# Kernel optimization log

Hardware: AMD Instinct MI355X
Metric: run time of the kernel (lower is better)

Reference implementation:

```python
import jax, jax.numpy as jnp
import numpy as np

IN_SIZE, OUT_SIZE, EDGE_SIZE = 32, 32, 16
NET_LAYERS = [128, 128]          # cfg.net_layers (hidden sizes of the edge MLP)
B, N_NEIGH = 10000, 20           # nodes x neighbors
E = B * N_NEIGH                  # total edges


def setup_inputs() -> dict:
    key = jax.random.key(0)
    ks = jax.random.split(key, 16)
    h_v = jax.random.normal(ks[0], (B, N_NEIGH), jnp.float32)
    h_w = jax.random.normal(ks[1], (B, IN_SIZE), jnp.float32)
    e_vw = jax.random.normal(ks[2], (E, EDGE_SIZE), jnp.float32)
    dims = [EDGE_SIZE] + NET_LAYERS + [IN_SIZE * OUT_SIZE]
    params = {}
    for i, (din, dout) in enumerate(zip(dims[:-1], dims[1:])):
        bound = 1.0 / np.sqrt(din)  # torch nn.Linear default init
        params[f"W{i}"] = jax.random.uniform(ks[3 + 2 * i], (dout, din), jnp.float32, -bound, bound)
        params[f"b{i}"] = jax.random.uniform(ks[4 + 2 * i], (dout,), jnp.float32, -bound, bound)
    return {"h_v": h_v, "h_w": h_w, "e_vw": e_vw, **params}


def reference(h_v, h_w, e_vw, W0, b0, W1, b1, W2, b2):
    # Edge MLP: edge_size -> 128 -> 128 -> in*out (ReLU on hidden layers only)
    x = jax.nn.relu(e_vw @ W0.T + b0)
    x = jax.nn.relu(x @ W1.T + b1)
    m = (x @ W2.T + b2).reshape(-1, OUT_SIZE, IN_SIZE)  # [E, out, in]

    # Faithful reproduction of h_w[..., None].expand(B, in, n).view(-1, in)
    n = h_v.shape[1]
    h_w_rows = jnp.broadcast_to(h_w[:, :, None], (h_w.shape[0], IN_SIZE, n)).reshape(-1, IN_SIZE)  # [E, in]

    # bmm(m, h_w_rows[..., None]).squeeze() -> [E, out]
    out = jnp.einsum("eoi,ei->eo", m, h_w_rows)
    return jnp.squeeze(out)
```

## Files before the change

kernel.cpp:

```cpp
#include <hip/hip_runtime.h>


typedef __bf16 bf16x8 __attribute__((ext_vector_type(8)));
typedef float  f32x4  __attribute__((ext_vector_type(4)));

#define NB       10000
#define NNEIGH   20
#define PADH     136
#define NCHUNK   25

#define WS_W0S   0
#define WS_W1B   8192
#define WS_W2G   40960
#define WS_B2G   532480
#define WS_HWG   540160

__device__ __forceinline__ unsigned short f2bf(float f) {
    unsigned int u = __float_as_uint(f);
    unsigned int r = (u + 0x7fffu + ((u >> 16) & 1u)) >> 16;
    return (unsigned short)r;
}
__device__ __forceinline__ unsigned int pack2(float a, float b) {
    return (unsigned int)f2bf(a) | ((unsigned int)f2bf(b) << 16);
}

__global__ __launch_bounds__(256) void prep_kernel(
    const float* __restrict__ W0, const float* __restrict__ b0,
    const float* __restrict__ W1,
    const float* __restrict__ W2, const float* __restrict__ b2,
    const float* __restrict__ h_w,
    unsigned short* __restrict__ w0s, unsigned short* __restrict__ w1b,
    unsigned short* __restrict__ w2g, float* __restrict__ b2g,
    float* __restrict__ hwg)
{
    const int bx = blockIdx.x, tid = threadIdx.x;
    if (bx < 16) {
        int gid = bx * 256 + tid;
        int o = gid >> 7, k = gid & 127;
        float pref[32];
        float run = 0.f;
#pragma unroll
        for (int i = 0; i < 32; ++i) {
            run += W2[(size_t)(32 * o + i) * 128 + k];
            pref[i] = run;
        }
#pragma unroll
        for (int kn = 0; kn < 20; ++kn) {
            const int j0 = (32 * kn) / 20;
#pragma unroll
            for (int g = 0; g < 3; ++g) {
                int lo = 20 * (j0 + g) - 32 * kn;     if (lo < 0) lo = 0;
                int hi = 20 * (j0 + g + 1) - 32 * kn; if (hi > 32) hi = 32;
                float v = (hi > lo) ? (pref[hi - 1] - (lo > 0 ? pref[lo - 1] : 0.f)) : 0.f;
                w2g[((size_t)(kn * 3 + g) * 32 + o) * 128 + k] = f2bf(v);
            }
        }
    } else if (bx == 16) {
        for (int t = 0; t < 16; ++t) {
            int idx = t * 256 + tid;
            int ct = idx >> 9, lane = (idx >> 3) & 63, j = idx & 7;
            int lq = lane & 15, q = lane >> 4;
            int k = q * 8 + j, o = ct * 16 + lq;
            float v = (k < 16) ? W0[o * 16 + k] : (k == 16 ? b0[o] : 0.f);
            w0s[idx] = f2bf(v);
        }
    } else if (bx <= 32) {
        int base = (bx - 17) * 1024;
        for (int i2 = tid; i2 < 1024; i2 += 256)
            w1b[base + i2] = f2bf(W1[base + i2]);
    } else if (bx == 33) {
        for (int idx = tid; idx < 1920; idx += 256) {
            int kn = idx / 96, rem = idx - kn * 96;
            int g = rem >> 5, o = rem & 31;
            int j0 = (32 * kn) / 20;
            int lo = 20 * (j0 + g) - 32 * kn;     if (lo < 0) lo = 0;
            int hi = 20 * (j0 + g + 1) - 32 * kn; if (hi > 32) hi = 32;
            float s = 0.f;
            for (int i = lo; i < hi; ++i) s += b2[32 * o + i];
            b2g[idx] = s;
        }
    } else {
#pragma unroll
        for (int t = 0; t < 4; ++t) {
            int idx = (bx - 34) * 1024 + t * 256 + tid;
            if (idx < 600000) {
                int kn3 = idx / 10000, b = idx - kn3 * 10000;
                int kn = kn3 / 3, g = kn3 - kn * 3;
                int jv = (32 * kn) / 20 + g; if (jv > 31) jv = 31;
                hwg[idx] = h_w[b * 32 + jv];
            }
        }
    }
}

__global__ __launch_bounds__(256) void msg_kernel(
    const float* __restrict__ hwg, const float* __restrict__ e_vw,
    const float* __restrict__ b1v,
    const unsigned short* __restrict__ w0s, const unsigned short* __restrict__ w1b,
    const unsigned short* __restrict__ w2g, const float* __restrict__ b2g,
    float* __restrict__ out)
{
    __shared__ __align__(16) unsigned short sW1[128 * PADH];
    __shared__ __align__(16) unsigned short sW2g[96 * PADH];
    __shared__ __align__(16) unsigned short sX[64 * PADH];
    __shared__ __align__(16) float sB1[128];
    __shared__ __align__(16) float sB2G[96];

    const int tid = threadIdx.x;
    const int lane = tid & 63, w = tid >> 6;
    const int quad = lane >> 4, lq = lane & 15;
    const int kn = blockIdx.y, chunk = blockIdx.x;
    const bool three = ((32 * kn) % 20) > 8;

    {
        const uint4* src = (const uint4*)w1b;
        uint4* dst = (uint4*)sW1;
        for (int i = tid; i < 2048; i += 256) { int r = i >> 4, c = i & 15; dst[r * 17 + c] = src[i]; }
    }
    {
        const int n4 = three ? 1536 : 1024;
        const uint4* src = (const uint4*)(w2g + (size_t)kn * 96 * 128);
        uint4* dst = (uint4*)sW2g;
        for (int i = tid; i < n4; i += 256) { int r = i >> 4, c = i & 15; dst[r * 17 + c] = src[i]; }
    }
    if (tid < 128) sB1[tid] = b1v[tid];
    if (tid < 96)  sB2G[tid] = b2g[kn * 96 + tid];

    bf16x8 w0f[8];
#pragma unroll
    for (int ct = 0; ct < 8; ++ct)
        w0f[ct] = *(const bf16x8*)(w0s + (ct * 64 + lane) * 8);
    __syncthreads();

    const int rbase = w * 16;
    const unsigned short one_bf = 0x3f80;

    float4 f0, f1;
    float hwv[3];
    {
        const int e = chunk * 64 + rbase + lq;
        if (quad < 2 && e < NB) {
            const float4* p = (const float4*)(e_vw + ((size_t)e * NNEIGH + kn) * 16 + quad * 8);
            f0 = p[0]; f1 = p[1];
        }
        hwv[0] = (e < NB) ? hwg[(kn * 3 + 0) * NB + e] : 0.f;
        hwv[1] = (e < NB) ? hwg[(kn * 3 + 1) * NB + e] : 0.f;
        hwv[2] = (three && e < NB) ? hwg[(kn * 3 + 2) * NB + e] : 0.f;
    }

    for (int btile = chunk; btile < 157; btile += NCHUNK) {
        const int e = btile * 64 + rbase + lq;

        union { bf16x8 v; uint4 u; } B;
        B.u = make_uint4(0u, 0u, 0u, 0u);
        if (quad < 2) {
            if (e < NB)
                B.u = make_uint4(pack2(f0.x, f0.y), pack2(f0.z, f0.w),
                                 pack2(f1.x, f1.y), pack2(f1.z, f1.w));
        } else if (quad == 2) {
            B.u.x = (unsigned int)one_bf;
        }
        float hw0 = hwv[0], hw1 = hwv[1], hw2 = hwv[2];

        {
            const int ne = (btile + NCHUNK) * 64 + rbase + lq;
            if (btile + NCHUNK < 157) {
                if (quad < 2 && ne < NB) {
                    const float4* p = (const float4*)(e_vw + ((size_t)ne * NNEIGH + kn) * 16 + quad * 8);
                    f0 = p[0]; f1 = p[1];
                }
                hwv[0] = (ne < NB) ? hwg[(kn * 3 + 0) * NB + ne] : 0.f;
                hwv[1] = (ne < NB) ? hwg[(kn * 3 + 1) * NB + ne] : 0.f;
                hwv[2] = (three && ne < NB) ? hwg[(kn * 3 + 2) * NB + ne] : 0.f;
            }
        }

#pragma unroll
        for (int ct = 0; ct < 8; ++ct) {
            f32x4 acc = {0.f, 0.f, 0.f, 0.f};
            acc = __builtin_amdgcn_mfma_f32_16x16x32_bf16(w0f[ct], B.v, acc, 0, 0, 0);
#pragma unroll
            for (int r2 = 0; r2 < 4; ++r2) acc[r2] = acc[r2] > 0.f ? acc[r2] : 0.f;
            uint2 pk = make_uint2(pack2(acc[0], acc[1]), pack2(acc[2], acc[3]));
            *(uint2*)&sX[(rbase + lq) * PADH + ct * 16 + quad * 4] = pk;
        }

        {
            bf16x8 xf[4];
#pragma unroll
            for (int ka = 0; ka < 4; ++ka)
                xf[ka] = *(const bf16x8*)&sX[(rbase + lq) * PADH + ka * 32 + quad * 8];
#pragma unroll
            for (int ct = 0; ct < 8; ++ct) {
                f32x4 acc = *(const f32x4*)&sB1[ct * 16 + quad * 4];
#pragma unroll
                for (int ka = 0; ka < 4; ++ka) {
                    bf16x8 wf = *(const bf16x8*)&sW1[(ct * 16 + lq) * PADH + ka * 32 + quad * 8];
                    acc = __builtin_amdgcn_mfma_f32_16x16x32_bf16(wf, xf[ka], acc, 0, 0, 0);
                }
#pragma unroll
                for (int r2 = 0; r2 < 4; ++r2) acc[r2] = acc[r2] > 0.f ? acc[r2] : 0.f;
                uint2 pk = make_uint2(pack2(acc[0], acc[1]), pack2(acc[2], acc[3]));
                *(uint2*)&sX[(rbase + lq) * PADH + ct * 16 + quad * 4] = pk;
            }
        }

        {
            bf16x8 xf[4];
#pragma unroll
            for (int ka = 0; ka < 4; ++ka)
                xf[ka] = *(const bf16x8*)&sX[(rbase + lq) * PADH + ka * 32 + quad * 8];
            f32x4 accC[6];
#pragma unroll
            for (int ct = 0; ct < 4; ++ct) {
                f32x4 acc = *(const f32x4*)&sB2G[ct * 16 + quad * 4];
#pragma unroll
                for (int ka = 0; ka < 4; ++ka) {
                    bf16x8 wf = *(const bf16x8*)&sW2g[(ct * 16 + lq) * PADH + ka * 32 + quad * 8];
                    acc = __builtin_amdgcn_mfma_f32_16x16x32_bf16(wf, xf[ka], acc, 0, 0, 0);
                }
                accC[ct] = acc;
            }
            if (three) {
#pragma unroll
                for (int ct = 4; ct < 6; ++ct) {
                    f32x4 acc = *(const f32x4*)&sB2G[ct * 16 + quad * 4];
#pragma unroll
                    for (int ka = 0; ka < 4; ++ka) {
                        bf16x8 wf = *(const bf16x8*)&sW2g[(ct * 16 + lq) * PADH + ka * 32 + quad * 8];
                        acc = __builtin_amdgcn_mfma_f32_16x16x32_bf16(wf, xf[ka], acc, 0, 0, 0);
                    }
                    accC[ct] = acc;
                }
            }
            if (e < NB) {
#pragma unroll
                for (int half = 0; half < 2; ++half) {
                    float4 val;
                    float* vp = &val.x;
#pragma unroll
                    for (int r2 = 0; r2 < 4; ++r2) {
                        float s = hw0 * accC[half][r2] + hw1 * accC[2 + half][r2];
                        if (three) s += hw2 * accC[4 + half][r2];
                        vp[r2] = s;
                    }
                    *(float4*)(out + ((size_t)e * NNEIGH + kn) * 32 + half * 16 + quad * 4) = val;
                }
            }
        }
    }
}

extern "C" void kernel_launch(void* const* d_in, const int* in_sizes, int n_in,
                              void* d_out, int out_size, void* d_ws, size_t ws_size,
                              hipStream_t stream)
{
    const float* h_w = (const float*)d_in[1];
    const float* e_vw = (const float*)d_in[2];
    const float* W0 = (const float*)d_in[3];
    const float* b0 = (const float*)d_in[4];
    const float* W1 = (const float*)d_in[5];
    const float* b1 = (const float*)d_in[6];
    const float* W2 = (const float*)d_in[7];
    const float* b2 = (const float*)d_in[8];
    float* out = (float*)d_out;

    char* ws = (char*)d_ws;
    unsigned short* w0s = (unsigned short*)(ws + WS_W0S);
    unsigned short* w1b = (unsigned short*)(ws + WS_W1B);
    unsigned short* w2g = (unsigned short*)(ws + WS_W2G);
    float*          b2g = (float*)(ws + WS_B2G);
    float*          hwg = (float*)(ws + WS_HWG);

    prep_kernel<<<34 + 586, 256, 0, stream>>>(W0, b0, W1, W2, b2, h_w,
                                              w0s, w1b, w2g, b2g, hwg);
    dim3 grid(NCHUNK, 20);
    msg_kernel<<<grid, 256, 0, stream>>>(hwg, e_vw, b1, w0s, w1b, w2g, b2g, out);
}
```

Baseline: 133.0 us.

## Read layer-3 weights directly from global in MFMA fragment order, drop LDS staging

```diff
diff --git a/kernel.cpp b/kernel.cpp
--- a/kernel.cpp
+++ b/kernel.cpp
@@ -7,11 +7,11 @@
 #define NB       10000
 #define NNEIGH   20
 #define PADH     136
-#define NCHUNK   25
+#define NCHUNK   39
 
 #define WS_W0S   0
 #define WS_W1B   8192
-#define WS_W2G   40960
+#define WS_W2GS  40960
 #define WS_B2G   532480
 #define WS_HWG   540160
 
@@ -30,13 +30,14 @@
     const float* __restrict__ W2, const float* __restrict__ b2,
     const float* __restrict__ h_w,
     unsigned short* __restrict__ w0s, unsigned short* __restrict__ w1b,
-    unsigned short* __restrict__ w2g, float* __restrict__ b2g,
+    unsigned short* __restrict__ w2gs, float* __restrict__ b2g,
     float* __restrict__ hwg)
 {
     const int bx = blockIdx.x, tid = threadIdx.x;
     if (bx < 16) {
         int gid = bx * 256 + tid;
         int o = gid >> 7, k = gid & 127;
+        const int ka = k >> 5, quad = (k >> 3) & 3, j = k & 7;
         float pref[32];
         float run = 0.f;
 #pragma unroll
@@ -52,7 +53,10 @@
                 int lo = 20 * (j0 + g) - 32 * kn;     if (lo < 0) lo = 0;
                 int hi = 20 * (j0 + g + 1) - 32 * kn; if (hi > 32) hi = 32;
                 float v = (hi > lo) ? (pref[hi - 1] - (lo > 0 ? pref[lo - 1] : 0.f)) : 0.f;
-                w2g[((size_t)(kn * 3 + g) * 32 + o) * 128 + k] = f2bf(v);
+                int c = g * 32 + o;
+                int ct = c >> 4, lq = c & 15;
+                int lane = quad * 16 + lq;
+                w2gs[(size_t)(((kn * 6 + ct) * 4 + ka) * 64 + lane) * 8 + j] = f2bf(v);
             }
         }
     } else if (bx == 16) {
@@ -97,11 +101,10 @@
     const float* __restrict__ hwg, const float* __restrict__ e_vw,
     const float* __restrict__ b1v,
     const unsigned short* __restrict__ w0s, const unsigned short* __restrict__ w1b,
-    const unsigned short* __restrict__ w2g, const float* __restrict__ b2g,
+    const unsigned short* __restrict__ w2gs, const float* __restrict__ b2g,
     float* __restrict__ out)
 {
     __shared__ __align__(16) unsigned short sW1[128 * PADH];
-    __shared__ __align__(16) unsigned short sW2g[96 * PADH];
     __shared__ __align__(16) unsigned short sX[64 * PADH];
     __shared__ __align__(16) float sB1[128];
     __shared__ __align__(16) float sB2G[96];
@@ -117,12 +120,6 @@
         uint4* dst = (uint4*)sW1;
         for (int i = tid; i < 2048; i += 256) { int r = i >> 4, c = i & 15; dst[r * 17 + c] = src[i]; }
     }
-    {
-        const int n4 = three ? 1536 : 1024;
-        const uint4* src = (const uint4*)(w2g + (size_t)kn * 96 * 128);
-        uint4* dst = (uint4*)sW2g;
-        for (int i = tid; i < n4; i += 256) { int r = i >> 4, c = i & 15; dst[r * 17 + c] = src[i]; }
-    }
     if (tid < 128) sB1[tid] = b1v[tid];
     if (tid < 96)  sB2G[tid] = b2g[kn * 96 + tid];
 
@@ -134,6 +131,7 @@
 
     const int rbase = w * 16;
     const unsigned short one_bf = 0x3f80;
+    const unsigned short* w2base = w2gs + (size_t)kn * 6 * 4 * 512 + lane * 8;
 
     float4 f0, f1;
     float hwv[3];
@@ -213,10 +211,11 @@
             f32x4 accC[6];
 #pragma unroll
             for (int ct = 0; ct < 4; ++ct) {
+                const unsigned short* wp = w2base + (size_t)ct * 4 * 512;
                 f32x4 acc = *(const f32x4*)&sB2G[ct * 16 + quad * 4];
 #pragma unroll
                 for (int ka = 0; ka < 4; ++ka) {
-                    bf16x8 wf = *(const bf16x8*)&sW2g[(ct * 16 + lq) * PADH + ka * 32 + quad * 8];
+                    bf16x8 wf = *(const bf16x8*)(wp + ka * 512);
                     acc = __builtin_amdgcn_mfma_f32_16x16x32_bf16(wf, xf[ka], acc, 0, 0, 0);
                 }
                 accC[ct] = acc;
@@ -224,10 +223,11 @@
             if (three) {
 #pragma unroll
                 for (int ct = 4; ct < 6; ++ct) {
+                    const unsigned short* wp = w2base + (size_t)ct * 4 * 512;
                     f32x4 acc = *(const f32x4*)&sB2G[ct * 16 + quad * 4];
 #pragma unroll
                     for (int ka = 0; ka < 4; ++ka) {
-                        bf16x8 wf = *(const bf16x8*)&sW2g[(ct * 16 + lq) * PADH + ka * 32 + quad * 8];
+                        bf16x8 wf = *(const bf16x8*)(wp + ka * 512);
                         acc = __builtin_amdgcn_mfma_f32_16x16x32_bf16(wf, xf[ka], acc, 0, 0, 0);
                     }
                     accC[ct] = acc;
@@ -266,14 +266,14 @@
     float* out = (float*)d_out;
 
     char* ws = (char*)d_ws;
-    unsigned short* w0s = (unsigned short*)(ws + WS_W0S);
-    unsigned short* w1b = (unsigned short*)(ws + WS_W1B);
-    unsigned short* w2g = (unsigned short*)(ws + WS_W2G);
-    float*          b2g = (float*)(ws + WS_B2G);
-    float*          hwg = (float*)(ws + WS_HWG);
+    unsigned short* w0s  = (unsigned short*)(ws + WS_W0S);
+    unsigned short* w1b  = (unsigned short*)(ws + WS_W1B);
+    unsigned short* w2gs = (unsigned short*)(ws + WS_W2GS);
+    float*          b2g  = (float*)(ws + WS_B2G);
+    float*          hwg  = (float*)(ws + WS_HWG);
 
     prep_kernel<<<34 + 586, 256, 0, stream>>>(W0, b0, W1, W2, b2, h_w,
-                                              w0s, w1b, w2g, b2g, hwg);
+                                              w0s, w1b, w2gs, b2g, hwg);
     dim3 grid(NCHUNK, 20);
-    msg_kernel<<<grid, 256, 0, stream>>>(hwg, e_vw, b1, w0s, w1b, w2g, b2g, out);
-}
+    msg_kernel<<<grid, 256, 0, stream>>>(hwg, e_vw, b1, w0s, w1b, w2gs, b2g, out);
+}
```

Result: slower. 137.2 us (+3.2%).
